# Performance work log

Hardware: AMD Instinct MI355X
Metric: run time of the kernel (lower is better)

Reference implementation:

```python
import jax, jax.numpy as jnp
import numpy as np

N_NODES = 100000
D = 128
E_ER = 800000
E_EE = 800000
E_RR = 400000


def setup_inputs() -> dict:
    key = jax.random.key(0)
    ks = jax.random.split(key, 16)
    def lin(kw, kb, out_d, in_d):
        s = 1.0 / np.sqrt(in_d)
        w = jax.random.uniform(kw, (out_d, in_d), minval=-s, maxval=s, dtype=jnp.float32)
        b = jax.random.uniform(kb, (out_d,), minval=-s, maxval=s, dtype=jnp.float32)
        return w, b
    W_attn_w, W_attn_b = lin(ks[0], ks[1], D, 2 * D)
    w0_w, w0_b = lin(ks[2], ks[3], 1, D)
    W1_w, W1_b = lin(ks[4], ks[5], D, D)
    W2_w, W2_b = lin(ks[6], ks[7], D, D)
    W3_w, W3_b = lin(ks[8], ks[9], D, D)
    return {
        "node_emb": jax.random.normal(ks[10], (N_NODES, D), dtype=jnp.float32),
        "er_src": jax.random.randint(ks[11], (E_ER,), 0, N_NODES),
        "er_dst": jax.random.randint(ks[12], (E_ER,), 0, N_NODES),
        "ee_src": jax.random.randint(ks[13], (E_EE,), 0, N_NODES),
        "ee_dst": jax.random.randint(ks[14], (E_EE,), 0, N_NODES),
        "ee_weight": jax.random.uniform(ks[15], (E_EE,), dtype=jnp.float32),
        "rr_src": jax.random.randint(jax.random.fold_in(key, 100), (E_RR,), 0, N_NODES),
        "rr_dst": jax.random.randint(jax.random.fold_in(key, 101), (E_RR,), 0, N_NODES),
        "W_attn_w": W_attn_w, "W_attn_b": W_attn_b,
        "w0_w": w0_w, "w0_b": w0_b,
        "W1_w": W1_w, "W1_b": W1_b,
        "W2_w": W2_w, "W2_b": W2_b,
        "W3_w": W3_w, "W3_b": W3_b,
    }


def _segment_softmax(values, segment_ids, num_segments):
    # torch version: seg_max initialized to zeros with include_self=True -> max(0, seg max)
    seg_max = jnp.maximum(jax.ops.segment_max(values, segment_ids, num_segments=num_segments), 0.0)
    exp_v = jnp.exp(values - seg_max[segment_ids])
    seg_sum = jax.ops.segment_sum(exp_v, segment_ids, num_segments=num_segments)
    return exp_v / (seg_sum[segment_ids] + 1e-9)


def reference(node_emb, er_src, er_dst, ee_src, ee_dst, ee_weight, rr_src, rr_dst,
              W_attn_w, W_attn_b, w0_w, w0_b, W1_w, W1_b, W2_w, W2_b, W3_w, W3_b):
    N = node_emb.shape[0]
    # --- attention aggregation over er edges (entity <- relation) ---
    h_emb = node_emb[er_src]            # (E, D)
    r_emb = node_emb[er_dst]            # (E, D)
    pair = jnp.concatenate([r_emb, h_emb], axis=-1)  # (E, 2D)
    e_ij = (jnp.tanh(pair @ W_attn_w.T + W_attn_b) @ w0_w.T + w0_b)[:, 0]  # (E,)
    attn = _segment_softmax(e_ij, er_src, N)
    attn_agg = jax.ops.segment_sum(attn[:, None] * r_emb, er_src, num_segments=N)
    # --- mean aggregation ---
    mean_agg = jax.ops.segment_sum(h_emb, er_dst, num_segments=N)
    mean_cnt = jax.ops.segment_sum(jnp.ones_like(er_dst, dtype=node_emb.dtype), er_dst, num_segments=N)
    w = ee_weight[:, None]
    mean_agg = mean_agg + jax.ops.segment_sum(w * node_emb[ee_dst], ee_src, num_segments=N)
    mean_cnt = mean_cnt + jax.ops.segment_sum(ee_weight, ee_src, num_segments=N)
    mean_agg = mean_agg + jax.ops.segment_sum(node_emb[rr_dst], rr_src, num_segments=N)
    mean_cnt = mean_cnt + jax.ops.segment_sum(jnp.ones_like(rr_src, dtype=node_emb.dtype), rr_src, num_segments=N)
    mean_agg = mean_agg / jnp.clip(mean_cnt, 1.0, None)[:, None]
    return (jnp.tanh(node_emb @ W1_w.T + W1_b)
            + jnp.tanh(attn_agg @ W2_w.T + W2_b)
            + jnp.tanh(mean_agg @ W3_w.T + W3_b))
```

## Files before the change

kernel.cpp:

```cpp
#include <hip/hip_runtime.h>

typedef unsigned int u32;
typedef unsigned short u16;

#define D 128

typedef __attribute__((ext_vector_type(8))) short bf16x8;
typedef __attribute__((ext_vector_type(4))) float f32x4;
#define MFMA16x16(a, b, c) __builtin_amdgcn_mfma_f32_16x16x32_bf16(a, b, c, 0, 0, 0)

__device__ inline float b2f(u32 h) { return __uint_as_float((h & 0xffffu) << 16); }
__device__ inline u16 f2b(float f) {
    u32 u = __float_as_uint(f);
    return (u16)((u + 0x7fffu + ((u >> 16) & 1u)) >> 16);
}
__device__ inline float tanh_fast(float x) {
    x = fminf(fmaxf(x, -15.f), 15.f);
    float e = __expf(2.f * x);
    return (e - 1.f) * __builtin_amdgcn_rcpf(e + 1.f);
}


__global__ __launch_bounds__(256) void k_bhist(const int* __restrict__ er_src,
                                               const int* __restrict__ er_dst,
                                               const int* __restrict__ ee_src,
                                               const int* __restrict__ rr_src,
                                               int* __restrict__ histA,
                                               int* __restrict__ histM,
                                               int E_ER, int E_EE, int E_RR, int NBK) {
    __shared__ int hA[1024], hM[1024];
    int tid = threadIdx.x;
    for (int j = tid; j < NBK; j += 256) { hA[j] = 0; hM[j] = 0; }
    __syncthreads();
    int E_T = 2 * E_ER + E_EE + E_RR;
    int stride = gridDim.x * 256;
    for (int e = blockIdx.x * 256 + tid; e < E_T; e += stride) {
        int i = e;
        if (i < E_ER) { atomicAdd(&hA[er_src[i] >> 7], 1); continue; }
        i -= E_ER;
        int key;
        if (i < E_ER) key = er_dst[i];
        else {
            i -= E_ER;
            key = (i < E_EE) ? ee_src[i] : rr_src[i - E_EE];
        }
        atomicAdd(&hM[key >> 7], 1);
    }
    __syncthreads();
    for (int j = tid; j < NBK; j += 256) {
        histA[j * 256 + blockIdx.x] = hA[j];
        histM[j * 256 + blockIdx.x] = hM[j];
    }
}

__global__ void k_scan1_dual(const int* __restrict__ cnt2, int n,
                             int* __restrict__ off_src, int* __restrict__ off_mean,
                             int* __restrict__ bsum, int nbs) {
    __shared__ int sh[256];
    int b = blockIdx.x;
    const int* cnt = cnt2;
    int* out = off_src;
    int* bs = bsum;
    if (b >= nbs) { b -= nbs; cnt = cnt2 + n; out = off_mean; bs = bsum + 256; }
    int t = threadIdx.x;
    int base = b * 1024 + t * 4;
    int v0 = (base < n) ? cnt[base] : 0;
    int v1 = (base + 1 < n) ? cnt[base + 1] : 0;
    int v2 = (base + 2 < n) ? cnt[base + 2] : 0;
    int v3 = (base + 3 < n) ? cnt[base + 3] : 0;
    int s4 = v0 + v1 + v2 + v3;
    sh[t] = s4;
    __syncthreads();
    for (int o = 1; o < 256; o <<= 1) {
        int x = (t >= o) ? sh[t - o] : 0;
        __syncthreads();
        sh[t] += x;
        __syncthreads();
    }
    int p = sh[t] - s4;
    if (t == 255) bs[b] = sh[255];
    if (base < n) out[base] = p;
    p += v0;
    if (base + 1 < n) out[base + 1] = p;
    p += v1;
    if (base + 2 < n) out[base + 2] = p;
    p += v2;
    if (base + 3 < n) out[base + 3] = p;
}

__global__ void k_scan2_dual(int* __restrict__ bsum, int nb,
                             int* __restrict__ totA, int* __restrict__ totB) {
    __shared__ int sh[256];
    int* bs = bsum + blockIdx.x * 256;
    int* tot = blockIdx.x ? totB : totA;
    int t = threadIdx.x;
    int v = (t < nb) ? bs[t] : 0;
    sh[t] = v;
    __syncthreads();
    for (int o = 1; o < 256; o <<= 1) {
        int x = (t >= o) ? sh[t - o] : 0;
        __syncthreads();
        sh[t] += x;
        __syncthreads();
    }
    if (t < nb) bs[t] = sh[t] - v;
    if (t == 255) *tot = sh[255];
}

__global__ void k_scan3b(int* __restrict__ offA, int* __restrict__ offM,
                         const int* __restrict__ bsum, int n) {
    int i = blockIdx.x * 256 + threadIdx.x;
    if (i < n) offA[i] += bsum[i >> 10];
    else if (i < 2 * n) offM[i - n] += bsum[256 + ((i - n) >> 10)];
}

__global__ __launch_bounds__(256) void k_bin(const int* __restrict__ er_src,
                                             const int* __restrict__ er_dst,
                                             const int* __restrict__ ee_src,
                                             const int* __restrict__ ee_dst,
                                             const int* __restrict__ rr_src,
                                             const int* __restrict__ rr_dst,
                                             const float* __restrict__ ee_w,
                                             const int* __restrict__ offA,
                                             const int* __restrict__ offM,
                                             int* __restrict__ recA,
                                             int2* __restrict__ recM,
                                             int E_ER, int E_EE, int E_RR, int NBK) {
    __shared__ int cA[1024], cM[1024];
    int tid = threadIdx.x, blk = blockIdx.x;
    for (int j = tid; j < NBK; j += 256) {
        cA[j] = offA[j * 256 + blk];
        cM[j] = offM[j * 256 + blk];
    }
    __syncthreads();
    int E_T = 2 * E_ER + E_EE + E_RR;
    int stride = gridDim.x * 256;
    for (int e = blk * 256 + tid; e < E_T; e += stride) {
        int i = e;
        if (i < E_ER) {
            int key = er_src[i];
            int p = atomicAdd(&cA[key >> 7], 1);
            recA[p] = er_dst[i] | ((key & 127) << 17);
            continue;
        }
        i -= E_ER;
        int sct, gat;
        float w;
        if (i < E_ER) {
            sct = er_dst[i]; gat = er_src[i]; w = 1.f;
        } else {
            i -= E_ER;
            if (i < E_EE) { sct = ee_src[i]; gat = ee_dst[i]; w = ee_w[i]; }
            else { i -= E_EE; sct = rr_src[i]; gat = rr_dst[i]; w = 1.f; }
        }
        int p = atomicAdd(&cM[sct >> 7], 1);
        recM[p] = make_int2(gat | ((sct & 127) << 17), __float_as_int(w));
    }
}

__global__ __launch_bounds__(256) void k_bucket(const int* __restrict__ offA_h,
                                                const int* __restrict__ offM_h,
                                                const int* __restrict__ recA,
                                                const int2* __restrict__ recM,
                                                int* __restrict__ off_src,
                                                int* __restrict__ off_mean,
                                                int* __restrict__ er_lst,
                                                int2* __restrict__ gpack,
                                                int E_ER, int E_M, int N, int NBK) {
    __shared__ int cnt[256];
    __shared__ int scanbuf[256];
    __shared__ int cur[256];
    int b = blockIdx.x, tid = threadIdx.x;
    int a0 = offA_h[b * 256];
    int a1 = (b + 1 < NBK) ? offA_h[(b + 1) * 256] : E_ER;
    int m0 = offM_h[b * 256];
    int m1 = (b + 1 < NBK) ? offM_h[(b + 1) * 256] : E_M;
    cnt[tid] = 0;
    __syncthreads();
    for (int i = a0 + tid; i < a1; i += 256) atomicAdd(&cnt[(recA[i] >> 17) & 127], 1);
    for (int i = m0 + tid; i < m1; i += 256) atomicAdd(&cnt[128 + ((recM[i].x >> 17) & 127)], 1);
    __syncthreads();
    int v = cnt[tid];
    scanbuf[tid] = v;
    __syncthreads();
    for (int o = 1; o < 128; o <<= 1) {
        int x = ((tid & 127) >= o) ? scanbuf[tid - o] : 0;
        __syncthreads();
        scanbuf[tid] += x;
        __syncthreads();
    }
    int excl = scanbuf[tid] - v;
    int pos = ((tid < 128) ? a0 : m0) + excl;
    cur[tid] = pos;
    int node = b * 128 + (tid & 127);
    if (node < N) {
        if (tid < 128) off_src[node] = pos;
        else off_mean[node] = pos;
    }
    if (b == 0 && tid == 0) { off_src[N] = E_ER; off_mean[N] = E_M; }
    __syncthreads();
    for (int i = a0 + tid; i < a1; i += 256) {
        int r = recA[i];
        int p = atomicAdd(&cur[(r >> 17) & 127], 1);
        er_lst[p] = r & 0x1FFFF;
    }
    for (int i = m0 + tid; i < m1; i += 256) {
        int2 r = recM[i];
        int p = atomicAdd(&cur[128 + ((r.x >> 17) & 127)], 1);
        gpack[p] = make_int2(r.x & 0x1FFFF, r.y);
    }
}

__global__ void k_cast4(const float* __restrict__ src, u16* __restrict__ dst, int n4) {
    int i = blockIdx.x * 256 + threadIdx.x;
    if (i >= n4) return;
    float4 v = ((const float4*)src)[i];
    ushort4 o;
    o.x = f2b(v.x); o.y = f2b(v.y); o.z = f2b(v.z); o.w = f2b(v.w);
    ((ushort4*)dst)[i] = o;
}

__global__ void k_cast_w(const float* __restrict__ Wattn,
                         const float* __restrict__ W1, const float* __restrict__ W2,
                         const float* __restrict__ W3,
                         u16* __restrict__ Wcat, u16* __restrict__ W123h) {
    int i = blockIdx.x * 256 + threadIdx.x;
    if (i < 32768) {
        int dd = i >> 7, k = i & 127;
        float v = (dd < 128) ? Wattn[(size_t)dd * 256 + k]
                             : Wattn[(size_t)(dd - 128) * 256 + 128 + k];
        Wcat[i] = f2b(v);
        return;
    }
    i -= 32768;
    if (i < 16384) { W123h[i] = f2b(W1[i]); return; }
    i -= 16384;
    if (i < 16384) { W123h[16384 + i] = f2b(W2[i]); return; }
    i -= 16384;
    if (i < 16384) W123h[32768 + i] = f2b(W3[i]);
}

__global__ __launch_bounds__(256) void k_precompute_mfma(const u16* __restrict__ embh,
                                                         const u16* __restrict__ Wcat,
                                                         u16* __restrict__ A, int N) {
    __shared__ u16 sX[64][136];
    int nb = blockIdx.x * 64;
    int tid = threadIdx.x;
    for (int i = tid; i < 1024; i += 256) {
        int row = i >> 4, c8 = i & 15;
        int n = nb + row;
        uint4 v = make_uint4(0u, 0u, 0u, 0u);
        if (n < N) v = *(const uint4*)(embh + (size_t)n * 128 + c8 * 8);
        *(uint4*)&sX[row][c8 * 8] = v;
    }
    __syncthreads();
    int wid = tid >> 6, lane = tid & 63;
    int quad = lane >> 4, l15 = lane & 15;
#pragma unroll
    for (int ns = 0; ns < 4; ns++) {
        int dbase = (wid * 4 + ns) * 16;
        bf16x8 b[4];
#pragma unroll
        for (int ks = 0; ks < 4; ks++)
            b[ks] = *(const bf16x8*)(Wcat + (size_t)(dbase + l15) * 128 + ks * 32 + quad * 8);
#pragma unroll
        for (int ms = 0; ms < 4; ms++) {
            f32x4 acc = {0.f, 0.f, 0.f, 0.f};
#pragma unroll
            for (int ks = 0; ks < 4; ks++) {
                bf16x8 a = *(const bf16x8*)&sX[ms * 16 + l15][ks * 32 + quad * 8];
                acc = MFMA16x16(a, b[ks], acc);
            }
#pragma unroll
            for (int r = 0; r < 4; r++) {
                int row = nb + ms * 16 + quad * 4 + r;
                if (row < N) A[(size_t)row * 256 + dbase + l15] = f2b(acc[r]);
            }
        }
    }
}

__global__ __launch_bounds__(256) void k_attn(const u16* __restrict__ A,
                                              const int* __restrict__ off,
                                              const int* __restrict__ lst,
                                              const u16* __restrict__ embh,
                                              const float* __restrict__ Wb,
                                              const float* __restrict__ w0w,
                                              const float* __restrict__ w0b,
                                              u16* __restrict__ attn_h, int N) {
    int node = blockIdx.x * 4 + (threadIdx.x >> 6);
    if (node >= N) return;
    int lane = threadIdx.x & 63;
    u32 ah = *(const u32*)(A + (size_t)node * 256 + 128 + 2 * lane);
    float ahx = b2f(ah), ahy = b2f(ah >> 16);
    float2 bb = *(const float2*)(Wb + 2 * lane);
    float2 ww = *(const float2*)(w0w + 2 * lane);
    float w0bias = w0b[0];
    int s0 = off[node], s1 = off[node + 1];
    float l = 0.f, ox = 0.f, oy = 0.f;
    int s = s0;
    for (; s + 2 <= s1; s += 2) {
        int d0 = lst[s], d1 = lst[s + 1];
        u32 ar0 = *(const u32*)(A + (size_t)d0 * 256 + 2 * lane);
        u32 ar1 = *(const u32*)(A + (size_t)d1 * 256 + 2 * lane);
        u32 ev0 = *(const u32*)(embh + (size_t)d0 * 128 + 2 * lane);
        u32 ev1 = *(const u32*)(embh + (size_t)d1 * 128 + 2 * lane);
        float p0 = tanh_fast(b2f(ar0) + ahx + bb.x) * ww.x +
                   tanh_fast(b2f(ar0 >> 16) + ahy + bb.y) * ww.y;
        float p1 = tanh_fast(b2f(ar1) + ahx + bb.x) * ww.x +
                   tanh_fast(b2f(ar1 >> 16) + ahy + bb.y) * ww.y;
#pragma unroll
        for (int o = 32; o; o >>= 1) {
            p0 += __shfl_xor(p0, o);
            p1 += __shfl_xor(p1, o);
        }
        float e0 = __expf(p0 + w0bias);
        float e1 = __expf(p1 + w0bias);
        l += e0 + e1;
        ox += e0 * b2f(ev0) + e1 * b2f(ev1);
        oy += e0 * b2f(ev0 >> 16) + e1 * b2f(ev1 >> 16);
    }
    if (s < s1) {
        int d0 = lst[s];
        u32 ar0 = *(const u32*)(A + (size_t)d0 * 256 + 2 * lane);
        u32 ev0 = *(const u32*)(embh + (size_t)d0 * 128 + 2 * lane);
        float p0 = tanh_fast(b2f(ar0) + ahx + bb.x) * ww.x +
                   tanh_fast(b2f(ar0 >> 16) + ahy + bb.y) * ww.y;
#pragma unroll
        for (int o = 32; o; o >>= 1) p0 += __shfl_xor(p0, o);
        float e0 = __expf(p0 + w0bias);
        l += e0;
        ox += e0 * b2f(ev0);
        oy += e0 * b2f(ev0 >> 16);
    }
    float inv = 1.f / (l + 1e-9f);
    u32 o = (u32)f2b(ox * inv) | ((u32)f2b(oy * inv) << 16);
    *(u32*)(attn_h + (size_t)node * 128 + 2 * lane) = o;
}

__global__ __launch_bounds__(256) void k_mean_g(const int* __restrict__ off,
                                                const int2* __restrict__ gpack,
                                                const u16* __restrict__ embh,
                                                u16* __restrict__ mean_h, int N) {
    int node = blockIdx.x * 4 + (threadIdx.x >> 6);
    if (node >= N) return;
    int lane = threadIdx.x & 63;
    int s0 = off[node], s1 = off[node + 1];
    float ax = 0.f, ay = 0.f, c = 0.f;
    int s = s0;
    for (; s + 4 <= s1; s += 4) {
        int2 p0 = gpack[s], p1 = gpack[s + 1], p2 = gpack[s + 2], p3 = gpack[s + 3];
        u32 v0 = *(const u32*)(embh + (size_t)p0.x * 128 + 2 * lane);
        u32 v1 = *(const u32*)(embh + (size_t)p1.x * 128 + 2 * lane);
        u32 v2 = *(const u32*)(embh + (size_t)p2.x * 128 + 2 * lane);
        u32 v3 = *(const u32*)(embh + (size_t)p3.x * 128 + 2 * lane);
        float w0 = __int_as_float(p0.y), w1 = __int_as_float(p1.y);
        float w2 = __int_as_float(p2.y), w3 = __int_as_float(p3.y);
        ax += w0 * b2f(v0) + w1 * b2f(v1) + w2 * b2f(v2) + w3 * b2f(v3);
        ay += w0 * b2f(v0 >> 16) + w1 * b2f(v1 >> 16) + w2 * b2f(v2 >> 16) + w3 * b2f(v3 >> 16);
        c += w0 + w1 + w2 + w3;
    }
    for (; s < s1; ++s) {
        int2 p0 = gpack[s];
        u32 v0 = *(const u32*)(embh + (size_t)p0.x * 128 + 2 * lane);
        float w0 = __int_as_float(p0.y);
        ax += w0 * b2f(v0);
        ay += w0 * b2f(v0 >> 16);
        c += w0;
    }
    c = c > 1.f ? c : 1.f;
    float inv = 1.f / c;
    u32 o = (u32)f2b(ax * inv) | ((u32)f2b(ay * inv) << 16);
    *(u32*)(mean_h + (size_t)node * 128 + 2 * lane) = o;
}

__global__ __launch_bounds__(256) void k_final_mfma(const u16* __restrict__ embh,
                                                    const u16* __restrict__ attn_h,
                                                    const u16* __restrict__ mean_h,
                                                    const u16* __restrict__ W123h,
                                                    const float* __restrict__ b1,
                                                    const float* __restrict__ b2,
                                                    const float* __restrict__ b3,
                                                    float* __restrict__ out, int N) {
    int nb = blockIdx.x * 64;
    int tid = threadIdx.x;
    int wid = tid >> 6, lane = tid & 63;
    int quad = lane >> 4, l15 = lane & 15;
    const u16* srcs[3] = {embh, attn_h, mean_h};
    const float* biases[3] = {b1, b2, b3};
#pragma unroll
    for (int ns = 0; ns < 2; ns++) {
        int d = (wid * 2 + ns) * 16 + l15;
        f32x4 res0 = {0.f, 0.f, 0.f, 0.f};
        f32x4 res1 = {0.f, 0.f, 0.f, 0.f};
        f32x4 res2 = {0.f, 0.f, 0.f, 0.f};
        f32x4 res3 = {0.f, 0.f, 0.f, 0.f};
#pragma unroll
        for (int arr = 0; arr < 3; arr++) {
            const u16* src = srcs[arr];
            bf16x8 b[4];
#pragma unroll
            for (int ks = 0; ks < 4; ks++)
                b[ks] = *(const bf16x8*)(W123h + (size_t)arr * 16384 +
                                         (size_t)d * 128 + ks * 32 + quad * 8);
            float bias = biases[arr][d];
#pragma unroll
            for (int ms = 0; ms < 4; ms++) {
                int row = nb + ms * 16 + l15;
                int rc = row < N ? row : N - 1;
                size_t rb = (size_t)rc * 128;
                f32x4 acc = {0.f, 0.f, 0.f, 0.f};
#pragma unroll
                for (int ks = 0; ks < 4; ks++) {
                    bf16x8 a = *(const bf16x8*)(src + rb + ks * 32 + quad * 8);
                    acc = MFMA16x16(a, b[ks], acc);
                }
                f32x4& res = (ms == 0) ? res0 : (ms == 1) ? res1 : (ms == 2) ? res2 : res3;
#pragma unroll
                for (int r = 0; r < 4; r++)
                    res[r] += tanh_fast(acc[r] + bias);
            }
        }
#pragma unroll
        for (int ms = 0; ms < 4; ms++) {
            f32x4& res = (ms == 0) ? res0 : (ms == 1) ? res1 : (ms == 2) ? res2 : res3;
#pragma unroll
            for (int r = 0; r < 4; r++) {
                int orow = nb + ms * 16 + quad * 4 + r;
                if (orow < N)
                    out[(size_t)orow * 128 + d] = res[r];
            }
        }
    }
}

extern "C" void kernel_launch(void* const* d_in, const int* in_sizes, int n_in,
                              void* d_out, int out_size, void* d_ws, size_t ws_size,
                              hipStream_t stream) {
    const float* emb     = (const float*)d_in[0];
    const int*   er_src  = (const int*)d_in[1];
    const int*   er_dst  = (const int*)d_in[2];
    const int*   ee_src  = (const int*)d_in[3];
    const int*   ee_dst  = (const int*)d_in[4];
    const float* ee_w    = (const float*)d_in[5];
    const int*   rr_src  = (const int*)d_in[6];
    const int*   rr_dst  = (const int*)d_in[7];
    const float* Wattn   = (const float*)d_in[8];
    const float* Wattn_b = (const float*)d_in[9];
    const float* w0w     = (const float*)d_in[10];
    const float* w0b     = (const float*)d_in[11];
    const float* W1      = (const float*)d_in[12];
    const float* b1      = (const float*)d_in[13];
    const float* W2      = (const float*)d_in[14];
    const float* b2      = (const float*)d_in[15];
    const float* W3      = (const float*)d_in[16];
    const float* b3      = (const float*)d_in[17];
    float* out = (float*)d_out;

    int N    = in_sizes[0] / D;
    int E_ER = in_sizes[1];
    int E_EE = in_sizes[3];
    int E_RR = in_sizes[6];
    int E_M  = E_ER + E_EE + E_RR;

    int NBK = (N + 127) >> 7;
    int HL  = NBK * 256;

    char* ws = (char*)d_ws;
    size_t off_b = 0;
    auto alloc = [&](size_t bytes) -> void* {
        void* p = ws + off_b;
        off_b += (bytes + 255) & ~(size_t)255;
        return p;
    };
    u16*   embh   = (u16*)alloc((size_t)N * 128 * 2);
    u16*   A      = (u16*)alloc((size_t)N * 256 * 2);
    u16*   mean_h = A;
    u16*   attn_h = (u16*)alloc((size_t)N * 128 * 2);
    u16*   Wcat_h = (u16*)alloc(256 * 128 * 2);
    u16*   W123h  = (u16*)alloc(3 * 128 * 128 * 2);
    int*   off_src  = (int*)alloc((size_t)(N + 1) * 4);
    int*   off_mean = (int*)alloc((size_t)(N + 1) * 4);
    int*   bsum     = (int*)alloc(514 * 4);
    int*   er_lst   = (int*)alloc((size_t)E_ER * 4);
    int2*  gpack    = (int2*)alloc((size_t)E_M * 8);

    char* Ab   = (char*)A;
    int2* recM = (int2*)Ab;
    int*  recA = (int*)(Ab + (size_t)E_M * 8);
    int*  hist2 = (int*)(Ab + (size_t)E_M * 8 + (size_t)E_ER * 4);
    int*  offHA = hist2 + 2 * HL;
    int*  offHM = offHA + HL;

    int nbh = (HL + 1023) / 1024;

    k_cast4<<<((N * 128 / 4) + 255) / 256, 256, 0, stream>>>(emb, embh, N * 128 / 4);
    k_cast_w<<<(81920 + 255) / 256, 256, 0, stream>>>(Wattn, W1, W2, W3, Wcat_h, W123h);

    k_bhist<<<256, 256, 0, stream>>>(er_src, er_dst, ee_src, rr_src,
                                     hist2, hist2 + HL, E_ER, E_EE, E_RR, NBK);
    k_scan1_dual<<<2 * nbh, 256, 0, stream>>>(hist2, HL, offHA, offHM, bsum, nbh);
    k_scan2_dual<<<2, 256, 0, stream>>>(bsum, nbh, bsum + 512, bsum + 513);
    k_scan3b<<<(2 * HL + 255) / 256, 256, 0, stream>>>(offHA, offHM, bsum, HL);
    k_bin<<<256, 256, 0, stream>>>(er_src, er_dst, ee_src, ee_dst, rr_src, rr_dst, ee_w,
                                   offHA, offHM, recA, recM, E_ER, E_EE, E_RR, NBK);
    k_bucket<<<NBK, 256, 0, stream>>>(offHA, offHM, recA, recM,
                                      off_src, off_mean, er_lst, gpack,
                                      E_ER, E_M, N, NBK);

    k_precompute_mfma<<<(N + 63) / 64, 256, 0, stream>>>(embh, Wcat_h, A, N);
    k_attn<<<(N + 3) / 4, 256, 0, stream>>>(A, off_src, er_lst, embh, Wattn_b, w0w, w0b,
                                            attn_h, N);
    k_mean_g<<<(N + 3) / 4, 256, 0, stream>>>(off_mean, gpack, embh, mean_h, N);
    k_final_mfma<<<(N + 63) / 64, 256, 0, stream>>>(embh, attn_h, mean_h, W123h,
                                                    b1, b2, b3, out, N);
}
```

Baseline: 544.2 us.

## Fuse attention, mean aggregation and final MFMA projection into one kernel

Merges the per-node attention softmax aggregation, the weighted mean gather and the final three-way MFMA projection into a single 512-thread kernel. Each block handles 64 nodes and stages the embedding, attention and mean rows in shared memory. The goal is to avoid writing attn_h and mean_h to global memory and reading them back, and to drop two kernel launches. In exchange, each wave now processes 8 nodes serially, so parallelism per node drops and the large shared-memory footprint (about 52KB) may limit occupancy.

Measured after the change: 533.0 us. 1.02x faster.

```diff
diff --git a/kernel.cpp b/kernel.cpp
--- a/kernel.cpp
+++ b/kernel.cpp
@@ -280,156 +280,152 @@
     }
 }
 
-__global__ __launch_bounds__(256) void k_attn(const u16* __restrict__ A,
-                                              const int* __restrict__ off,
-                                              const int* __restrict__ lst,
+__global__ __launch_bounds__(512) void k_fuse(const u16* __restrict__ A,
+                                              const int* __restrict__ offA,
+                                              const int* __restrict__ lstA,
+                                              const int* __restrict__ offM,
+                                              const int2* __restrict__ gpack,
                                               const u16* __restrict__ embh,
                                               const float* __restrict__ Wb,
                                               const float* __restrict__ w0w,
                                               const float* __restrict__ w0b,
-                                              u16* __restrict__ attn_h, int N) {
-    int node = blockIdx.x * 4 + (threadIdx.x >> 6);
-    if (node >= N) return;
-    int lane = threadIdx.x & 63;
-    u32 ah = *(const u32*)(A + (size_t)node * 256 + 128 + 2 * lane);
-    float ahx = b2f(ah), ahy = b2f(ah >> 16);
+                                              const u16* __restrict__ W123h,
+                                              const float* __restrict__ b1,
+                                              const float* __restrict__ b2,
+                                              const float* __restrict__ b3,
+                                              float* __restrict__ out, int N) {
+    __shared__ u16 sX[3][64][136];
+    int nb = blockIdx.x * 64;
+    int tid = threadIdx.x;
+    int wid = tid >> 6, lane = tid & 63;
+
+    for (int j = tid; j < 1024; j += 512) {
+        int row = j >> 4, c8 = j & 15;
+        int n = nb + row;
+        uint4 v = make_uint4(0u, 0u, 0u, 0u);
+        if (n < N) v = *(const uint4*)(embh + (size_t)n * 128 + c8 * 8);
+        *(uint4*)&sX[0][row][c8 * 8] = v;
+    }
+
     float2 bb = *(const float2*)(Wb + 2 * lane);
     float2 ww = *(const float2*)(w0w + 2 * lane);
     float w0bias = w0b[0];
-    int s0 = off[node], s1 = off[node + 1];
-    float l = 0.f, ox = 0.f, oy = 0.f;
-    int s = s0;
-    for (; s + 2 <= s1; s += 2) {
-        int d0 = lst[s], d1 = lst[s + 1];
-        u32 ar0 = *(const u32*)(A + (size_t)d0 * 256 + 2 * lane);
-        u32 ar1 = *(const u32*)(A + (size_t)d1 * 256 + 2 * lane);
-        u32 ev0 = *(const u32*)(embh + (size_t)d0 * 128 + 2 * lane);
-        u32 ev1 = *(const u32*)(embh + (size_t)d1 * 128 + 2 * lane);
-        float p0 = tanh_fast(b2f(ar0) + ahx + bb.x) * ww.x +
-                   tanh_fast(b2f(ar0 >> 16) + ahy + bb.y) * ww.y;
-        float p1 = tanh_fast(b2f(ar1) + ahx + bb.x) * ww.x +
-                   tanh_fast(b2f(ar1 >> 16) + ahy + bb.y) * ww.y;
-#pragma unroll
-        for (int o = 32; o; o >>= 1) {
-            p0 += __shfl_xor(p0, o);
-            p1 += __shfl_xor(p1, o);
-        }
-        float e0 = __expf(p0 + w0bias);
-        float e1 = __expf(p1 + w0bias);
-        l += e0 + e1;
-        ox += e0 * b2f(ev0) + e1 * b2f(ev1);
-        oy += e0 * b2f(ev0 >> 16) + e1 * b2f(ev1 >> 16);
-    }
-    if (s < s1) {
-        int d0 = lst[s];
-        u32 ar0 = *(const u32*)(A + (size_t)d0 * 256 + 2 * lane);
-        u32 ev0 = *(const u32*)(embh + (size_t)d0 * 128 + 2 * lane);
-        float p0 = tanh_fast(b2f(ar0) + ahx + bb.x) * ww.x +
-                   tanh_fast(b2f(ar0 >> 16) + ahy + bb.y) * ww.y;
-#pragma unroll
-        for (int o = 32; o; o >>= 1) p0 += __shfl_xor(p0, o);
-        float e0 = __expf(p0 + w0bias);
-        l += e0;
-        ox += e0 * b2f(ev0);
-        oy += e0 * b2f(ev0 >> 16);
-    }
-    float inv = 1.f / (l + 1e-9f);
-    u32 o = (u32)f2b(ox * inv) | ((u32)f2b(oy * inv) << 16);
-    *(u32*)(attn_h + (size_t)node * 128 + 2 * lane) = o;
-}
-
-__global__ __launch_bounds__(256) void k_mean_g(const int* __restrict__ off,
-                                                const int2* __restrict__ gpack,
-                                                const u16* __restrict__ embh,
-                                                u16* __restrict__ mean_h, int N) {
-    int node = blockIdx.x * 4 + (threadIdx.x >> 6);
-    if (node >= N) return;
-    int lane = threadIdx.x & 63;
-    int s0 = off[node], s1 = off[node + 1];
-    float ax = 0.f, ay = 0.f, c = 0.f;
-    int s = s0;
-    for (; s + 4 <= s1; s += 4) {
-        int2 p0 = gpack[s], p1 = gpack[s + 1], p2 = gpack[s + 2], p3 = gpack[s + 3];
-        u32 v0 = *(const u32*)(embh + (size_t)p0.x * 128 + 2 * lane);
-        u32 v1 = *(const u32*)(embh + (size_t)p1.x * 128 + 2 * lane);
-        u32 v2 = *(const u32*)(embh + (size_t)p2.x * 128 + 2 * lane);
-        u32 v3 = *(const u32*)(embh + (size_t)p3.x * 128 + 2 * lane);
-        float w0 = __int_as_float(p0.y), w1 = __int_as_float(p1.y);
-        float w2 = __int_as_float(p2.y), w3 = __int_as_float(p3.y);
-        ax += w0 * b2f(v0) + w1 * b2f(v1) + w2 * b2f(v2) + w3 * b2f(v3);
-        ay += w0 * b2f(v0 >> 16) + w1 * b2f(v1 >> 16) + w2 * b2f(v2 >> 16) + w3 * b2f(v3 >> 16);
-        c += w0 + w1 + w2 + w3;
-    }
-    for (; s < s1; ++s) {
-        int2 p0 = gpack[s];
-        u32 v0 = *(const u32*)(embh + (size_t)p0.x * 128 + 2 * lane);
-        float w0 = __int_as_float(p0.y);
-        ax += w0 * b2f(v0);
-        ay += w0 * b2f(v0 >> 16);
-        c += w0;
-    }
-    c = c > 1.f ? c : 1.f;
-    float inv = 1.f / c;
-    u32 o = (u32)f2b(ax * inv) | ((u32)f2b(ay * inv) << 16);
-    *(u32*)(mean_h + (size_t)node * 128 + 2 * lane) = o;
-}
-
-__global__ __launch_bounds__(256) void k_final_mfma(const u16* __restrict__ embh,
-                                                    const u16* __restrict__ attn_h,
-                                                    const u16* __restrict__ mean_h,
-                                                    const u16* __restrict__ W123h,
-                                                    const float* __restrict__ b1,
-                                                    const float* __restrict__ b2,
-                                                    const float* __restrict__ b3,
-                                                    float* __restrict__ out, int N) {
-    int nb = blockIdx.x * 64;
-    int tid = threadIdx.x;
-    int wid = tid >> 6, lane = tid & 63;
+    for (int i = 0; i < 8; ++i) {
+        int local = wid * 8 + i;
+        int node = nb + local;
+        if (node < N) {
+            u32 ah = *(const u32*)(A + (size_t)node * 256 + 128 + 2 * lane);
+            float ahx = b2f(ah), ahy = b2f(ah >> 16);
+            int s0 = offA[node], s1 = offA[node + 1];
+            float l = 0.f, ox = 0.f, oy = 0.f;
+            int s = s0;
+            for (; s + 2 <= s1; s += 2) {
+                int d0 = lstA[s], d1 = lstA[s + 1];
+                u32 ar0 = *(const u32*)(A + (size_t)d0 * 256 + 2 * lane);
+                u32 ar1 = *(const u32*)(A + (size_t)d1 * 256 + 2 * lane);
+                u32 ev0 = *(const u32*)(embh + (size_t)d0 * 128 + 2 * lane);
+                u32 ev1 = *(const u32*)(embh + (size_t)d1 * 128 + 2 * lane);
+                float p0 = tanh_fast(b2f(ar0) + ahx + bb.x) * ww.x +
+                           tanh_fast(b2f(ar0 >> 16) + ahy + bb.y) * ww.y;
+                float p1 = tanh_fast(b2f(ar1) + ahx + bb.x) * ww.x +
+                           tanh_fast(b2f(ar1 >> 16) + ahy + bb.y) * ww.y;
+#pragma unroll
+                for (int o = 32; o; o >>= 1) {
+                    p0 += __shfl_xor(p0, o);
+                    p1 += __shfl_xor(p1, o);
+                }
+                float e0 = __expf(p0 + w0bias);
+                float e1 = __expf(p1 + w0bias);
+                l += e0 + e1;
+                ox += e0 * b2f(ev0) + e1 * b2f(ev1);
+                oy += e0 * b2f(ev0 >> 16) + e1 * b2f(ev1 >> 16);
+            }
+            if (s < s1) {
+                int d0 = lstA[s];
+                u32 ar0 = *(const u32*)(A + (size_t)d0 * 256 + 2 * lane);
+                u32 ev0 = *(const u32*)(embh + (size_t)d0 * 128 + 2 * lane);
+                float p0 = tanh_fast(b2f(ar0) + ahx + bb.x) * ww.x +
+                           tanh_fast(b2f(ar0 >> 16) + ahy + bb.y) * ww.y;
+#pragma unroll
+                for (int o = 32; o; o >>= 1) p0 += __shfl_xor(p0, o);
+                float e0 = __expf(p0 + w0bias);
+                l += e0;
+                ox += e0 * b2f(ev0);
+                oy += e0 * b2f(ev0 >> 16);
+            }
+            float inv = 1.f / (l + 1e-9f);
+            *(u32*)&sX[1][local][2 * lane] =
+                (u32)f2b(ox * inv) | ((u32)f2b(oy * inv) << 16);
+
+            s0 = offM[node]; s1 = offM[node + 1];
+            float ax = 0.f, ay = 0.f, c = 0.f;
+            s = s0;
+            for (; s + 4 <= s1; s += 4) {
+                int2 p0 = gpack[s], p1 = gpack[s + 1], p2 = gpack[s + 2], p3 = gpack[s + 3];
+                u32 v0 = *(const u32*)(embh + (size_t)p0.x * 128 + 2 * lane);
+                u32 v1 = *(const u32*)(embh + (size_t)p1.x * 128 + 2 * lane);
+                u32 v2 = *(const u32*)(embh + (size_t)p2.x * 128 + 2 * lane);
+                u32 v3 = *(const u32*)(embh + (size_t)p3.x * 128 + 2 * lane);
+                float w0 = __int_as_float(p0.y), w1 = __int_as_float(p1.y);
+                float w2 = __int_as_float(p2.y), w3 = __int_as_float(p3.y);
+                ax += w0 * b2f(v0) + w1 * b2f(v1) + w2 * b2f(v2) + w3 * b2f(v3);
+                ay += w0 * b2f(v0 >> 16) + w1 * b2f(v1 >> 16) +
+                      w2 * b2f(v2 >> 16) + w3 * b2f(v3 >> 16);
+                c += w0 + w1 + w2 + w3;
+            }
+            for (; s < s1; ++s) {
+                int2 p0 = gpack[s];
+                u32 v0 = *(const u32*)(embh + (size_t)p0.x * 128 + 2 * lane);
+                float w0 = __int_as_float(p0.y);
+                ax += w0 * b2f(v0);
+                ay += w0 * b2f(v0 >> 16);
+                c += w0;
+            }
+            c = c > 1.f ? c : 1.f;
+            float minv = 1.f / c;
+            *(u32*)&sX[2][local][2 * lane] =
+                (u32)f2b(ax * minv) | ((u32)f2b(ay * minv) << 16);
+        }
+    }
+    __syncthreads();
+
     int quad = lane >> 4, l15 = lane & 15;
-    const u16* srcs[3] = {embh, attn_h, mean_h};
+    int d = wid * 16 + l15;
     const float* biases[3] = {b1, b2, b3};
-#pragma unroll
-    for (int ns = 0; ns < 2; ns++) {
-        int d = (wid * 2 + ns) * 16 + l15;
-        f32x4 res0 = {0.f, 0.f, 0.f, 0.f};
-        f32x4 res1 = {0.f, 0.f, 0.f, 0.f};
-        f32x4 res2 = {0.f, 0.f, 0.f, 0.f};
-        f32x4 res3 = {0.f, 0.f, 0.f, 0.f};
-#pragma unroll
-        for (int arr = 0; arr < 3; arr++) {
-            const u16* src = srcs[arr];
-            bf16x8 b[4];
-#pragma unroll
-            for (int ks = 0; ks < 4; ks++)
-                b[ks] = *(const bf16x8*)(W123h + (size_t)arr * 16384 +
-                                         (size_t)d * 128 + ks * 32 + quad * 8);
-            float bias = biases[arr][d];
-#pragma unroll
-            for (int ms = 0; ms < 4; ms++) {
-                int row = nb + ms * 16 + l15;
-                int rc = row < N ? row : N - 1;
-                size_t rb = (size_t)rc * 128;
-                f32x4 acc = {0.f, 0.f, 0.f, 0.f};
-#pragma unroll
-                for (int ks = 0; ks < 4; ks++) {
-                    bf16x8 a = *(const bf16x8*)(src + rb + ks * 32 + quad * 8);
-                    acc = MFMA16x16(a, b[ks], acc);
-                }
-                f32x4& res = (ms == 0) ? res0 : (ms == 1) ? res1 : (ms == 2) ? res2 : res3;
-#pragma unroll
-                for (int r = 0; r < 4; r++)
-                    res[r] += tanh_fast(acc[r] + bias);
-            }
-        }
+    f32x4 res0 = {0.f, 0.f, 0.f, 0.f};
+    f32x4 res1 = {0.f, 0.f, 0.f, 0.f};
+    f32x4 res2 = {0.f, 0.f, 0.f, 0.f};
+    f32x4 res3 = {0.f, 0.f, 0.f, 0.f};
+#pragma unroll
+    for (int arr = 0; arr < 3; arr++) {
+        bf16x8 b[4];
+#pragma unroll
+        for (int ks = 0; ks < 4; ks++)
+            b[ks] = *(const bf16x8*)(W123h + (size_t)arr * 16384 +
+                                     (size_t)d * 128 + ks * 32 + quad * 8);
+        float bias = biases[arr][d];
 #pragma unroll
         for (int ms = 0; ms < 4; ms++) {
+            f32x4 acc = {0.f, 0.f, 0.f, 0.f};
+#pragma unroll
+            for (int ks = 0; ks < 4; ks++) {
+                bf16x8 a = *(const bf16x8*)&sX[arr][ms * 16 + l15][ks * 32 + quad * 8];
+                acc = MFMA16x16(a, b[ks], acc);
+            }
             f32x4& res = (ms == 0) ? res0 : (ms == 1) ? res1 : (ms == 2) ? res2 : res3;
 #pragma unroll
-            for (int r = 0; r < 4; r++) {
-                int orow = nb + ms * 16 + quad * 4 + r;
-                if (orow < N)
-                    out[(size_t)orow * 128 + d] = res[r];
-            }
+            for (int r = 0; r < 4; r++)
+                res[r] += tanh_fast(acc[r] + bias);
+        }
+    }
+#pragma unroll
+    for (int ms = 0; ms < 4; ms++) {
+        f32x4& res = (ms == 0) ? res0 : (ms == 1) ? res1 : (ms == 2) ? res2 : res3;
+#pragma unroll
+        for (int r = 0; r < 4; r++) {
+            int orow = nb + ms * 16 + quad * 4 + r;
+            if (orow < N)
+                out[(size_t)orow * 128 + d] = res[r];
         }
     }
 }
@@ -475,8 +471,6 @@
     };
     u16*   embh   = (u16*)alloc((size_t)N * 128 * 2);
     u16*   A      = (u16*)alloc((size_t)N * 256 * 2);
-    u16*   mean_h = A;
-    u16*   attn_h = (u16*)alloc((size_t)N * 128 * 2);
     u16*   Wcat_h = (u16*)alloc(256 * 128 * 2);
     u16*   W123h  = (u16*)alloc(3 * 128 * 128 * 2);
     int*   off_src  = (int*)alloc((size_t)(N + 1) * 4);
@@ -509,9 +503,7 @@
                                       E_ER, E_M, N, NBK);
 
     k_precompute_mfma<<<(N + 63) / 64, 256, 0, stream>>>(embh, Wcat_h, A, N);
-    k_attn<<<(N + 3) / 4, 256, 0, stream>>>(A, off_src, er_lst, embh, Wattn_b, w0w, w0b,
-                                            attn_h, N);
-    k_mean_g<<<(N + 3) / 4, 256, 0, stream>>>(off_mean, gpack, embh, mean_h, N);
-    k_final_mfma<<<(N + 63) / 64, 256, 0, stream>>>(embh, attn_h, mean_h, W123h,
-                                                    b1, b2, b3, out, N);
-}
+    k_fuse<<<(N + 63) / 64, 512, 0, stream>>>(A, off_src, er_lst, off_mean, gpack,
+                                              embh, Wattn_b, w0w, w0b, W123h,
+                                              b1, b2, b3, out, N);
+}
```
